# Performance work log

Hardware: AMD Instinct MI355X
Metric: run time of the kernel (lower is better)

## Reference

```python
import jax, jax.numpy as jnp
import numpy as np

NUM_BINS = 32
SIGMA_RATIO = 0.5          # Gaussian Parzen window width relative to bin spacing
SMOOTH_NR = 1e-07
SMOOTH_DR = 1e-07


def setup_inputs() -> dict:
    key = jax.random.key(0)
    k1, k2 = jax.random.split(key)
    shape = (2, 1, 96, 96, 96)
    pred = jax.random.uniform(k1, shape, dtype=jnp.float32)
    target = jax.random.uniform(k2, shape, dtype=jnp.float32)
    return {"pred": pred, "target": target}


def _parzen_weights(img_flat, bin_centers, preterm):
    # img_flat: [B, N]; bin_centers: [nb]
    # Gaussian Parzen window, normalized so each voxel's weights sum to 1 over bins.
    d = img_flat[..., None] - bin_centers          # [B, N, nb]
    w = jnp.exp(-preterm * d * d)                  # [B, N, nb]
    return w / jnp.sum(w, axis=-1, keepdims=True)


def reference(pred, target):
    B = pred.shape[0]
    nb = NUM_BINS
    bin_centers = jnp.linspace(0.0, 1.0, nb, dtype=jnp.float32)  # [nb]
    bin_width = 1.0 / (nb - 1)
    sigma = SIGMA_RATIO * bin_width
    preterm = jnp.float32(1.0 / (2.0 * sigma * sigma))

    p = pred.reshape(B, -1)    # [B, N]
    t = target.reshape(B, -1)  # [B, N]
    N = p.shape[1]

    wa = _parzen_weights(p, bin_centers, preterm)  # [B, N, nb]
    wb = _parzen_weights(t, bin_centers, preterm)  # [B, N, nb]

    # joint histogram [B, nb, nb] and marginals [B, 1, nb]
    pab = jnp.einsum('bni,bnj->bij', wa, wb) / N
    pa = jnp.mean(wa, axis=1, keepdims=True).transpose(0, 2, 1).transpose(0, 2, 1)  # [B,1,nb]
    pa = jnp.mean(wa, axis=1)[:, None, :]  # [B, 1, nb]
    pb = jnp.mean(wb, axis=1)[:, None, :]  # [B, 1, nb]

    # papb = bmm(pa^T, pb): outer product of marginals -> [B, nb, nb]
    papb = jnp.einsum('bki,bkj->bij', pa, pb)

    mi = jnp.sum(pab * jnp.log((pab + SMOOTH_NR) / (papb + SMOOTH_DR) + SMOOTH_DR),
                 axis=(-1, -2))  # [B]
    return -jnp.mean(mi)
```

## Files before the change

kernel.cpp:

```cpp
#include <hip/hip_runtime.h>
#include <hip/hip_bf16.h>

#define NBINS 32
#define CHUNK 128
#define NROWS 34
#define STR 136
#define TILE_HALVES (NROWS * STR)
#define NTHREADS 256
#define NVOX 884736
#define BPB 512
#define NSLOTS 16

typedef __attribute__((ext_vector_type(8))) _Float16 half8;
typedef __attribute__((ext_vector_type(16))) float f32x16;
typedef __attribute__((ext_vector_type(4))) int i32x4;

__device__ __forceinline__ void compute_w(float x, int& kb, _Float16* wq) {
    float tt = x * 31.0f;
    float kf = rintf(tt);
    int ki = (int)kf;
    float u = tt - kf;
    kb = ki - 3 + (u > 0.0f ? 1 : 0);
    float w[6];
    float s = 0.0f;
#pragma unroll
    for (int o = 0; o < 6; ++o) {
        int b = kb + o;
        float d = tt - (float)b;
        float e = __expf(-2.0f * d * d);
        e = ((unsigned)b < NBINS) ? e : 0.0f;
        w[o] = e;
        s += e;
    }
    float rinv = 1.0f / s;
#pragma unroll
    for (int o = 0; o < 6; ++o) wq[o] = (_Float16)(w[o] * rinv);
}

__device__ __forceinline__ void scatter6_save(_Float16* __restrict__ L, int col, int kb,
                                              const _Float16* wq, int* adr) {
#pragma unroll
    for (int o = 0; o < 6; ++o) {
        int r = min(max(kb + o, -1), 32) + 1;
        int a = r * STR + col;
        adr[o] = a;
        L[a] = wq[o];
    }
}
__device__ __forceinline__ void zero6_adr(_Float16* __restrict__ L, const int* adr) {
#pragma unroll
    for (int o = 0; o < 6; ++o) L[adr[o]] = (_Float16)0.0f;
}

__global__ __launch_bounds__(NTHREADS, 4)
void mi_hist_kernel(const float* __restrict__ pred, const float* __restrict__ targ,
                    float* __restrict__ hist ) {
    __shared__ __attribute__((aligned(16))) _Float16 smem[4 * TILE_HALVES];

    const int tid = threadIdx.x;
    const int bx = blockIdx.x;
    const int batch = blockIdx.y;
    const int col = tid & 127;
    const bool isB = tid >= 128;
    const float* src = (isB ? targ : pred) + (size_t)batch * NVOX;
    const int toff = isB ? TILE_HALVES : 0;

    const int wid = tid >> 6;
    const int lane = tid & 63;
    const int frag = (1 + (lane & 31)) * STR + wid * 32 + 8 * (lane >> 5);

    float xs[14];
#pragma unroll
    for (int c = 0; c < 13; ++c)
        xs[c] = src[((size_t)(c * BPB + bx)) * CHUNK + col];
    const bool extra = (bx < 256);
    if (extra) xs[13] = src[((size_t)(13 * BPB + bx)) * CHUNK + col];

    {
        i32x4 z = {0, 0, 0, 0};
        i32x4* zp = (i32x4*)smem;
#pragma unroll
        for (int i = 0; i < 10; ++i) {
            int idx = i * NTHREADS + tid;
            if (idx < (4 * TILE_HALVES) / 8) zp[idx] = z;
        }
    }

    f32x16 acc;
#pragma unroll
    for (int r = 0; r < 16; ++r) acc[r] = 0.0f;

    int adr[2][6];

#define DO_MFMA(BASE) { \
        const _Float16* Pp = (BASE); \
        _Pragma("unroll") \
        for (int kk = 0; kk < 2; ++kk) { \
            half8 af = *(const half8*)&Pp[frag + kk * 16]; \
            half8 bf = *(const half8*)&Pp[TILE_HALVES + frag + kk * 16]; \
            acc = __builtin_amdgcn_mfma_f32_32x32x16_f16(af, bf, acc, 0, 0, 0); \
        } }

#pragma unroll
    for (int c = 0; c < 13; ++c) {
        _Float16 wq[6];
        int kb;
        compute_w(xs[c], kb, wq);
        __syncthreads();
        if (c >= 1) DO_MFMA(smem + (((c & 1) ^ 1) * 2) * TILE_HALVES);
        _Float16* cur = smem + (c & 1) * 2 * TILE_HALVES + toff;
        if (c >= 2) zero6_adr(cur, adr[c & 1]);
        scatter6_save(cur, col, kb, wq, adr[c & 1]);
    }
    if (extra) {
        _Float16 wq[6];
        int kb;
        compute_w(xs[13], kb, wq);
        __syncthreads();
        DO_MFMA(smem);
        _Float16* cur = smem + 2 * TILE_HALVES + toff;
        zero6_adr(cur, adr[1]);
        scatter6_save(cur, col, kb, wq, adr[1]);
        __syncthreads();
        DO_MFMA(smem + 2 * TILE_HALVES);
    } else {
        __syncthreads();
        DO_MFMA(smem);
    }
    __syncthreads();

    float* red = (float*)smem;
    const int colc = lane & 31;
    const int rlo = 4 * (lane >> 5);
#pragma unroll
    for (int r = 0; r < 16; ++r) {
        int rowc = (r & 3) + 8 * (r >> 2) + rlo;
        red[wid * 1024 + rowc * 32 + colc] = acc[r];
    }
    __syncthreads();
    float* H = hist + ((size_t)(bx & (NSLOTS - 1)) * 2 + batch) * 1024;
    for (int idx = tid; idx < 1024; idx += NTHREADS) {
        float s = red[idx] + red[1024 + idx] + red[2048 + idx] + red[3072 + idx];
        atomicAdd(&H[idx], s);
    }
}

__global__ void mi_reduce_kernel(const float* __restrict__ hist, float* __restrict__ out) {
    __shared__ float s_pab[2 * NBINS * NBINS];
    __shared__ double s_pa[2][NBINS];
    __shared__ double s_pb[2][NBINS];
    __shared__ double s_red[256];
    const int tid = threadIdx.x;
    const double invN = 1.0 / (double)NVOX;

    for (int g = tid; g < 512; g += 256) {
        float4 s = make_float4(0.f, 0.f, 0.f, 0.f);
        for (int sl = 0; sl < NSLOTS; ++sl) {
            float4 v = ((const float4*)hist)[sl * 512 + g];
            s.x += v.x; s.y += v.y; s.z += v.z; s.w += v.w;
        }
        ((float4*)s_pab)[g] = s;
    }
    __syncthreads();

    if (tid < 64) {
        int b = tid >> 5, i = tid & 31;
        double s = 0.0;
        for (int j = 0; j < NBINS; ++j) s += (double)s_pab[(b * NBINS + i) * NBINS + j];
        s_pa[b][i] = s * invN;
    } else if (tid < 128) {
        int t2 = tid - 64;
        int b = t2 >> 5, j = t2 & 31;
        double s = 0.0;
        for (int i = 0; i < NBINS; ++i) s += (double)s_pab[(b * NBINS + i) * NBINS + j];
        s_pb[b][j] = s * invN;
    }
    __syncthreads();

    double acc = 0.0;
    for (int idx = tid; idx < 2 * NBINS * NBINS; idx += 256) {
        int b = idx >> 10;
        int cell = idx & 1023;
        int i = cell >> 5, j = cell & 31;
        double pab = (double)s_pab[idx] * invN;
        double papb = s_pa[b][i] * s_pb[b][j];
        acc += pab * log((pab + 1e-7) / (papb + 1e-7) + 1e-7);
    }
    s_red[tid] = acc;
    __syncthreads();
    for (int s2 = 128; s2 > 0; s2 >>= 1) {
        if (tid < s2) s_red[tid] += s_red[tid + s2];
        __syncthreads();
    }
    if (tid == 0) out[0] = (float)(-0.5 * s_red[0]);
}

extern "C" void kernel_launch(void* const* d_in, const int* in_sizes, int n_in,
                              void* d_out, int out_size, void* d_ws, size_t ws_size,
                              hipStream_t stream) {
    const float* pred = (const float*)d_in[0];
    const float* targ = (const float*)d_in[1];
    float* hist = (float*)d_ws;
    float* out = (float*)d_out;

    hipMemsetAsync(hist, 0, NSLOTS * 2 * NBINS * NBINS * sizeof(float), stream);
    dim3 grid(BPB, 2);
    hipLaunchKernelGGL(mi_hist_kernel, grid, dim3(NTHREADS), 0, stream, pred, targ, hist);
    hipLaunchKernelGGL(mi_reduce_kernel, dim3(1), dim3(256), 0, stream, hist, out);
}
```

Before: 31.91 us.

## Give each wave private LDS tiles and drop block-wide barriers in histogram loop

```diff
diff --git a/kernel.cpp b/kernel.cpp
--- a/kernel.cpp
+++ b/kernel.cpp
@@ -2,10 +2,10 @@
 #include <hip/hip_bf16.h>
 
 #define NBINS 32
-#define CHUNK 128
+#define WSTR 66
 #define NROWS 34
-#define STR 136
-#define TILE_HALVES (NROWS * STR)
+#define WTILE (NROWS * WSTR)
+#define WAVE_LDS (2 * WTILE)
 #define NTHREADS 256
 #define NVOX 884736
 #define BPB 512
@@ -37,52 +37,59 @@
     for (int o = 0; o < 6; ++o) wq[o] = (_Float16)(w[o] * rinv);
 }
 
-__device__ __forceinline__ void scatter6_save(_Float16* __restrict__ L, int col, int kb,
+__device__ __forceinline__ void zero6_adr(_Float16* __restrict__ L, const int* adr) {
+#pragma unroll
+    for (int o = 0; o < 6; ++o) L[adr[o]] = (_Float16)0.0f;
+}
+__device__ __forceinline__ void scatter6_save(_Float16* __restrict__ L, int lane, int kb,
                                               const _Float16* wq, int* adr) {
 #pragma unroll
     for (int o = 0; o < 6; ++o) {
         int r = min(max(kb + o, -1), 32) + 1;
-        int a = r * STR + col;
+        int a = r * WSTR + lane;
         adr[o] = a;
         L[a] = wq[o];
     }
-}
-__device__ __forceinline__ void zero6_adr(_Float16* __restrict__ L, const int* adr) {
-#pragma unroll
-    for (int o = 0; o < 6; ++o) L[adr[o]] = (_Float16)0.0f;
 }
 
 __global__ __launch_bounds__(NTHREADS, 4)
 void mi_hist_kernel(const float* __restrict__ pred, const float* __restrict__ targ,
                     float* __restrict__ hist ) {
-    __shared__ __attribute__((aligned(16))) _Float16 smem[4 * TILE_HALVES];
+    __shared__ __attribute__((aligned(16))) _Float16 smem[4 * WAVE_LDS];
 
     const int tid = threadIdx.x;
     const int bx = blockIdx.x;
     const int batch = blockIdx.y;
-    const int col = tid & 127;
-    const bool isB = tid >= 128;
-    const float* src = (isB ? targ : pred) + (size_t)batch * NVOX;
-    const int toff = isB ? TILE_HALVES : 0;
-
     const int wid = tid >> 6;
     const int lane = tid & 63;
-    const int frag = (1 + (lane & 31)) * STR + wid * 32 + 8 * (lane >> 5);
-
-    float xs[14];
-#pragma unroll
-    for (int c = 0; c < 13; ++c)
-        xs[c] = src[((size_t)(c * BPB + bx)) * CHUNK + col];
-    const bool extra = (bx < 256);
-    if (extra) xs[13] = src[((size_t)(13 * BPB + bx)) * CHUNK + col];
+    _Float16* TA = smem + wid * WAVE_LDS;
+    _Float16* TB = TA + WTILE;
+    const float* p = pred + (size_t)batch * NVOX;
+    const float* t = targ + (size_t)batch * NVOX;
+
+    const int gw = bx * 4 + wid;
+    const bool seven = (bx < 384);
+
+    float xp[7], xt[7];
+#pragma unroll
+    for (int r = 0; r < 6; ++r) {
+        size_t off = ((size_t)(r * 2048 + gw)) * 64 + lane;
+        xp[r] = p[off];
+        xt[r] = t[off];
+    }
+    if (seven) {
+        size_t off = ((size_t)(6 * 2048 + gw)) * 64 + lane;
+        xp[6] = p[off];
+        xt[6] = t[off];
+    }
 
     {
         i32x4 z = {0, 0, 0, 0};
-        i32x4* zp = (i32x4*)smem;
-#pragma unroll
-        for (int i = 0; i < 10; ++i) {
-            int idx = i * NTHREADS + tid;
-            if (idx < (4 * TILE_HALVES) / 8) zp[idx] = z;
+        i32x4* zp = (i32x4*)TA;
+#pragma unroll
+        for (int i = 0; i < 9; ++i) {
+            int idx = i * 64 + lane;
+            if (idx < 561) zp[idx] = z;
         }
     }
 
@@ -90,43 +97,32 @@
 #pragma unroll
     for (int r = 0; r < 16; ++r) acc[r] = 0.0f;
 
-    int adr[2][6];
-
-#define DO_MFMA(BASE) { \
-        const _Float16* Pp = (BASE); \
+    int adrA[6], adrB[6];
+    const int frag = (1 + (lane & 31)) * WSTR + 8 * (lane >> 5);
+
+#define ROUND(R, ZO) { \
+        _Float16 wqA[6], wqB[6]; int kbA, kbB; \
+        compute_w(xp[R], kbA, wqA); \
+        compute_w(xt[R], kbB, wqB); \
+        if (ZO) { zero6_adr(TA, adrA); zero6_adr(TB, adrB); }    \
+        scatter6_save(TA, lane, kbA, wqA, adrA); \
+        scatter6_save(TB, lane, kbB, wqB, adrB); \
         _Pragma("unroll") \
-        for (int kk = 0; kk < 2; ++kk) { \
-            half8 af = *(const half8*)&Pp[frag + kk * 16]; \
-            half8 bf = *(const half8*)&Pp[TILE_HALVES + frag + kk * 16]; \
+        for (int m = 0; m < 4; ++m) { \
+            half8 af = *(const half8*)&TA[frag + 16 * m]; \
+            half8 bf = *(const half8*)&TB[frag + 16 * m]; \
             acc = __builtin_amdgcn_mfma_f32_32x32x16_f16(af, bf, acc, 0, 0, 0); \
         } }
 
-#pragma unroll
-    for (int c = 0; c < 13; ++c) {
-        _Float16 wq[6];
-        int kb;
-        compute_w(xs[c], kb, wq);
-        __syncthreads();
-        if (c >= 1) DO_MFMA(smem + (((c & 1) ^ 1) * 2) * TILE_HALVES);
-        _Float16* cur = smem + (c & 1) * 2 * TILE_HALVES + toff;
-        if (c >= 2) zero6_adr(cur, adr[c & 1]);
-        scatter6_save(cur, col, kb, wq, adr[c & 1]);
-    }
-    if (extra) {
-        _Float16 wq[6];
-        int kb;
-        compute_w(xs[13], kb, wq);
-        __syncthreads();
-        DO_MFMA(smem);
-        _Float16* cur = smem + 2 * TILE_HALVES + toff;
-        zero6_adr(cur, adr[1]);
-        scatter6_save(cur, col, kb, wq, adr[1]);
-        __syncthreads();
-        DO_MFMA(smem + 2 * TILE_HALVES);
-    } else {
-        __syncthreads();
-        DO_MFMA(smem);
-    }
+    ROUND(0, false)
+    ROUND(1, true)
+    ROUND(2, true)
+    ROUND(3, true)
+    ROUND(4, true)
+    ROUND(5, true)
+    if (seven) { ROUND(6, true) }
+#undef ROUND
+
     __syncthreads();
 
     float* red = (float*)smem;
```

Measured after the change: 50.91 us. 59.6% more time.
